# Kernel optimization log

Measured on AMD Instinct MI355X. Metric: run time of the kernel, lower is better.

Reference implementation:

```python
import jax, jax.numpy as jnp
import numpy as np
from jax import lax

K_NN = 16      # neighbors used by compute_knn_distance
ANCHOR_K = 64  # config['anchor_k']


def _knn_dist_vec(pts):
    """compute_knn_distance for one object: mean offset vector to K_NN nearest neighbors.
    pts: (N, 3) -> (N, 3)"""
    sq = jnp.sum(pts * pts, axis=-1)                      # (N,)
    d2 = sq[:, None] + sq[None, :] - 2.0 * (pts @ pts.T)  # (N, N) squared dists
    n = pts.shape[0]
    d2 = d2 + jnp.eye(n, dtype=pts.dtype) * 1e10          # exclude self
    _, idx = lax.top_k(-d2, K_NN)                          # (N, K_NN) nearest indices
    neigh = pts[idx]                                       # (N, K_NN, 3)
    return jnp.mean(neigh - pts[:, None, :], axis=1)       # (N, 3)


def _fps(pts, k):
    """Farthest point sampling for one object. pts: (N, 3) -> (k,) int32 indices."""
    d0 = jnp.sum((pts - pts[0]) ** 2, axis=-1)             # dist to seed point 0

    def step(min_d, _):
        idx = jnp.argmax(min_d)
        d = jnp.sum((pts - pts[idx]) ** 2, axis=-1)
        return jnp.minimum(min_d, d), idx

    _, idxs = lax.scan(step, d0, None, length=k - 1)
    return jnp.concatenate([jnp.zeros((1,), dtype=idxs.dtype), idxs])


def setup_inputs() -> dict:
    key = jax.random.key(0)
    k1, k2, k3, k4 = jax.random.split(key, 4)
    B, N_obj, N_v = 4, 8, 2048
    positions = jax.random.normal(k1, (B, N_obj, N_v, 3), dtype=jnp.float32)
    velocities = jax.random.normal(k2, (B, N_obj, N_v, 3), dtype=jnp.float32)
    physics_params = jax.random.uniform(k3, (B, N_obj, 3), dtype=jnp.float32)
    # reference pose at t=0: nearby but distinct so rel_pos is nontrivial
    ref_positions = positions + 0.05 * jax.random.normal(k4, (B, N_obj, N_v, 3), dtype=jnp.float32)
    return {"positions": positions, "velocities": velocities,
            "physics_params": physics_params, "ref_positions": ref_positions}


def reference(positions, velocities, physics_params, ref_positions):
    B, N_obj, N_v, _ = positions.shape
    flat = positions.reshape(B * N_obj, N_v, 3)

    # pairwise KNN distance feature per point
    dist_vec = jax.vmap(_knn_dist_vec)(flat).reshape(B, N_obj, N_v, 3)

    # iterative FPS anchor sampling (vectorized over all B*N_obj objects)
    anchors = jax.vmap(lambda p: _fps(p, ANCHOR_K))(flat).reshape(B, N_obj, ANCHOR_K)

    rel_pos = positions - ref_positions

    # multi-field gather at anchor indices (torch.gather on dim=2)
    gather = lambda f: jnp.take_along_axis(f, anchors[..., None], axis=2)
    anchor_dist = gather(dist_vec)       # (B, N_obj, K, 3)
    anchor_vel = gather(velocities)      # (B, N_obj, K, 3)
    anchor_rel = gather(rel_pos)         # (B, N_obj, K, 3)

    phys = jnp.broadcast_to(physics_params[:, :, None, :], (B, N_obj, ANCHOR_K, 3))
    query = jnp.concatenate([anchor_dist, anchor_vel, anchor_rel, phys], axis=-1)  # (B, N_obj, K, 12)
    return query
```

## Files before the change

kernel.cpp:

```cpp
#include <hip/hip_runtime.h>
#include <stdint.h>

#define NPTS 2048
#define KNN  16
#define AK   64
#define TPB  256
#define FPT  8
#define FPP  4
#define KPL  32
#define KPP  16

typedef unsigned long long u64;
typedef unsigned int u32;
typedef __attribute__((ext_vector_type(2))) float v2f;
#define UMAX 0xFFFFFFFFFFFFFFFFull

__device__ __forceinline__ float sq3(float x, float y, float z) {
    return __fadd_rn(__fadd_rn(__fmul_rn(x, x), __fmul_rn(y, y)), __fmul_rn(z, z));
}

template <int CTRL, int RMASK>
__device__ __forceinline__ u32 dpp32(u32 v) {
    return (u32)__builtin_amdgcn_update_dpp((int)v, (int)v, CTRL, RMASK, 0xF, false);
}

#define FMAX_STEP(CTRL, RMASK) \
    m = fmaxf(m, __uint_as_float(dpp32<CTRL, RMASK>(__float_as_uint(m))))
#define UMIN_STEP(CTRL, RMASK) \
    { const u32 o_ = dpp32<CTRL, RMASK>(c); c = (o_ < c) ? o_ : c; }

__device__ __forceinline__ float wave_fmax(float m) {
    FMAX_STEP(0xB1, 0xF);
    FMAX_STEP(0x4E, 0xF);
    FMAX_STEP(0x141, 0xF);
    FMAX_STEP(0x140, 0xF);
    FMAX_STEP(0x142, 0xA);
    FMAX_STEP(0x143, 0xC);
    return __uint_as_float((u32)__builtin_amdgcn_readlane(
        (int)__float_as_uint(m), 63));
}

__device__ __forceinline__ u32 wave_umin(u32 c) {
    UMIN_STEP(0xB1, 0xF);
    UMIN_STEP(0x4E, 0xF);
    UMIN_STEP(0x141, 0xF);
    UMIN_STEP(0x140, 0xF);
    UMIN_STEP(0x142, 0xA);
    UMIN_STEP(0x143, 0xC);
    return (u32)__builtin_amdgcn_readlane((int)c, 63);
}

template <int CTRL, int RMASK>
__device__ __forceinline__ u64 minstep(u64 k) {
    const u32 olo = dpp32<CTRL, RMASK>((u32)k);
    const u32 ohi = dpp32<CTRL, RMASK>((u32)(k >> 32));
    const u64 o = ((u64)ohi << 32) | olo;
    return (o < k) ? o : k;
}

__device__ __forceinline__ u64 wave_min64(u64 k) {
    k = minstep<0xB1, 0xF>(k);
    k = minstep<0x4E, 0xF>(k);
    k = minstep<0x141, 0xF>(k);
    k = minstep<0x140, 0xF>(k);
    k = minstep<0x142, 0xA>(k);
    k = minstep<0x143, 0xC>(k);
    const u32 lo = (u32)__builtin_amdgcn_readlane((int)(u32)k, 63);
    const u32 hi = (u32)__builtin_amdgcn_readlane((int)(u32)(k >> 32), 63);
    return ((u64)hi << 32) | lo;
}

__global__ __launch_bounds__(TPB) void fps_kernel(const float* __restrict__ pos,
                                                  int* __restrict__ anchors) {
#pragma clang fp contract(off)
    const int obj = blockIdx.x;
    const int t = threadIdx.x;
    const int wid = t >> 6;
    const float* pts = pos + (size_t)obj * NPTS * 3;

    __shared__ u64 skey[8];
    __shared__ float4 scrd[8];

    v2f px[FPP], py[FPP], pz[FPP], mind[FPP];
    float bv, bx, by, bz;
    u32 bj;
    {
        const float ax0 = pts[0], ay0 = pts[1], az0 = pts[2];
        bv = -1.0f; bj = 0; bx = by = bz = 0.0f;
        #pragma unroll
        for (int i = 0; i < FPP; i++) {
            const int jA = t + (2 * i) * TPB;
            const int jB = t + (2 * i + 1) * TPB;
            v2f X, Y, Z;
            X.x = pts[jA * 3 + 0]; Y.x = pts[jA * 3 + 1]; Z.x = pts[jA * 3 + 2];
            X.y = pts[jB * 3 + 0]; Y.y = pts[jB * 3 + 1]; Z.y = pts[jB * 3 + 2];
            px[i] = X; py[i] = Y; pz[i] = Z;
            const v2f dx = X - ax0, dy = Y - ay0, dz = Z - az0;
            const v2f d2 = dx * dx + dy * dy + dz * dz;
            mind[i] = d2;
            if (d2.x > bv) { bv = d2.x; bj = (u32)jA; bx = X.x; by = Y.x; bz = Z.x; }
            if (d2.y > bv) { bv = d2.y; bj = (u32)jB; bx = X.y; by = Y.y; bz = Z.y; }
        }
    }
    if (t == 0) anchors[obj * AK + 0] = 0;

    for (int s = 1; s < AK; s++) {
        const float wmax = wave_fmax(bv);
        const u32 cand = (bv == wmax) ? bj : 0xFFFFFFFFu;
        const u32 wj = wave_umin(cand);

        const int side = (s & 1) * 4;
        if (bv == wmax && bj == wj) {
            skey[side + wid] = ((u64)__float_as_uint(wmax) << 32) | (u32)(~wj);
            scrd[side + wid] = make_float4(bx, by, bz, 0.0f);
        }
        __syncthreads();

        u64 ka = skey[side + 0];
        float4 ca = scrd[side + 0];
        { const u64 kb = skey[side + 1]; const float4 cb = scrd[side + 1];
          if (kb > ka) { ka = kb; ca = cb; } }
        { const u64 kb = skey[side + 2]; const float4 cb = scrd[side + 2];
          if (kb > ka) { ka = kb; ca = cb; } }
        { const u64 kb = skey[side + 3]; const float4 cb = scrd[side + 3];
          if (kb > ka) { ka = kb; ca = cb; } }
        if (t == 0) anchors[obj * AK + s] = (int)(~(u32)ka);
        if (s == AK - 1) break;

        bv = -1.0f; bj = 0;
        #pragma unroll
        for (int i = 0; i < FPP; i++) {
            const v2f dx = px[i] - ca.x, dy = py[i] - ca.y, dz = pz[i] - ca.z;
            const v2f d2 = dx * dx + dy * dy + dz * dz;
            v2f nm;
            nm.x = fminf(mind[i].x, d2.x);
            nm.y = fminf(mind[i].y, d2.y);
            mind[i] = nm;
            if (nm.x > bv) { bv = nm.x; bj = (u32)(t + (2 * i) * TPB);
                             bx = px[i].x; by = py[i].x; bz = pz[i].x; }
            if (nm.y > bv) { bv = nm.y; bj = (u32)(t + (2 * i + 1) * TPB);
                             bx = px[i].y; by = py[i].y; bz = pz[i].y; }
        }
    }
}

__global__ __launch_bounds__(TPB) void knn_gather_kernel(
    const float* __restrict__ pos, const float* __restrict__ vel,
    const float* __restrict__ phys, const float* __restrict__ refp,
    const int* __restrict__ anchors, float* __restrict__ out) {
#pragma clang fp contract(off)
    const int t = threadIdx.x;
    const int wid = t >> 6, lane = t & 63;
    const int g = blockIdx.x * 4 + wid;
    const int obj = g >> 6;

    __shared__ float sX[NPTS], sY[NPTS], sZ[NPTS];
    const float* pts = pos + (size_t)obj * NPTS * 3;
    #pragma unroll
    for (int i = 0; i < FPT; i++) {
        const int j = t + i * TPB;
        sX[j] = pts[j * 3 + 0];
        sY[j] = pts[j * 3 + 1];
        sZ[j] = pts[j * 3 + 2];
    }
    const int a = anchors[g];
    __syncthreads();

    const float ax = sX[a], ay = sY[a], az = sZ[a];
    const float sqa = sq3(ax, ay, az);

    u64 k[KPL];
    #pragma unroll
    for (int i = 0; i < KPP; i++) {
        const int jA = lane + (2 * i) * 64, jB = lane + (2 * i + 1) * 64;
        v2f X, Y, Z;
        X.x = sX[jA]; Y.x = sY[jA]; Z.x = sZ[jA];
        X.y = sX[jB]; Y.y = sY[jB]; Z.y = sZ[jB];
        const v2f sqj = X * X + Y * Y + Z * Z;
        const v2f dot = ax * X + ay * Y + az * Z;
        const v2f d2 = (sqa + sqj) - 2.0f * dot;
        u32 b0 = __float_as_uint(d2.x);
        b0 ^= (b0 & 0x80000000u) ? 0xFFFFFFFFu : 0x80000000u;
        u32 b1 = __float_as_uint(d2.y);
        b1 ^= (b1 & 0x80000000u) ? 0xFFFFFFFFu : 0x80000000u;
        k[2 * i]     = (jA == a) ? UMAX : (((u64)b0 << 32) | (u32)jA);
        k[2 * i + 1] = (jB == a) ? UMAX : (((u64)b1 << 32) | (u32)jB);
    }

    u64 c0 = UMAX, c1 = UMAX;
    #pragma unroll
    for (int i = 0; i < KPL; i++) c0 = (k[i] < c0) ? k[i] : c0;
    #pragma unroll
    for (int i = 0; i < KPL; i++) {
        const u64 v = (k[i] > c0) ? k[i] : UMAX; c1 = (v < c1) ? v : c1;
    }

    float accx = 0.f, accy = 0.f, accz = 0.f;
    u64 thr = 0;
    for (int r = 0; r < KNN; r++) {
        if (c0 == UMAX) {
            #pragma unroll
            for (int i = 0; i < KPL; i++) {
                const u64 v = (k[i] > thr) ? k[i] : UMAX; c0 = (v < c0) ? v : c0;
            }
            #pragma unroll
            for (int i = 0; i < KPL; i++) {
                const u64 v = (k[i] > c0) ? k[i] : UMAX; c1 = (v < c1) ? v : c1;
            }
        }
        const u64 w = wave_min64(c0);
        const int winj = (int)(u32)w;
        accx = __fadd_rn(accx, __fsub_rn(sX[winj], ax));
        accy = __fadd_rn(accy, __fsub_rn(sY[winj], ay));
        accz = __fadd_rn(accz, __fsub_rn(sZ[winj], az));
        if (c0 == w) {
            thr = c0; c0 = c1; c1 = UMAX;
        }
    }

    if (lane == 0) {
        float* o = out + (size_t)g * 12;
        o[0] = __fmul_rn(accx, 0.0625f);
        o[1] = __fmul_rn(accy, 0.0625f);
        o[2] = __fmul_rn(accz, 0.0625f);
        const size_t base = (size_t)obj * NPTS * 3 + (size_t)a * 3;
        o[3] = vel[base + 0];
        o[4] = vel[base + 1];
        o[5] = vel[base + 2];
        o[6] = __fsub_rn(pos[base + 0], refp[base + 0]);
        o[7] = __fsub_rn(pos[base + 1], refp[base + 1]);
        o[8] = __fsub_rn(pos[base + 2], refp[base + 2]);
        const float* ph = phys + (size_t)obj * 3;
        o[9]  = ph[0];
        o[10] = ph[1];
        o[11] = ph[2];
    }
}

extern "C" void kernel_launch(void* const* d_in, const int* in_sizes, int n_in,
                              void* d_out, int out_size, void* d_ws, size_t ws_size,
                              hipStream_t stream) {
    const float* pos  = (const float*)d_in[0];
    const float* vel  = (const float*)d_in[1];
    const float* phys = (const float*)d_in[2];
    const float* refp = (const float*)d_in[3];
    float* out = (float*)d_out;

    const int n_obj = in_sizes[2] / 3;
    int* anchors = (int*)d_ws;

    fps_kernel<<<n_obj, TPB, 0, stream>>>(pos, anchors);
    knn_gather_kernel<<<n_obj * AK / 4, TPB, 0, stream>>>(pos, vel, phys, refp,
                                                          anchors, out);
}
```

Baseline: 117.4 us.

## Run FPS with one wavefront per object, removing block-level barriers

The FPS kernel now uses a single 64-lane wave per object, so each lane holds 32 points in registers instead of 8. The per-step cross-wave argmax through shared memory and __syncthreads is replaced by pure wave reductions. The winning point's coordinates are fetched with readlane from whichever register slot holds them. This removes barrier and LDS latency from the 63 serial steps. In exchange each step does four times more distance work per lane on four times fewer threads, and register pressure rises.

```diff
diff --git a/kernel.cpp b/kernel.cpp
--- a/kernel.cpp
+++ b/kernel.cpp
@@ -6,7 +6,6 @@
 #define AK   64
 #define TPB  256
 #define FPT  8
-#define FPP  4
 #define KPL  32
 #define KPP  16
 
@@ -70,27 +69,27 @@
     return ((u64)hi << 32) | lo;
 }
 
-__global__ __launch_bounds__(TPB) void fps_kernel(const float* __restrict__ pos,
-                                                  int* __restrict__ anchors) {
+__device__ __forceinline__ float rdlane(float v, u32 l) {
+    return __uint_as_float(
+        (u32)__builtin_amdgcn_readlane((int)__float_as_uint(v), (int)l));
+}
+
+__global__ __launch_bounds__(64) void fps_kernel(const float* __restrict__ pos,
+                                                 int* __restrict__ anchors) {
 #pragma clang fp contract(off)
     const int obj = blockIdx.x;
-    const int t = threadIdx.x;
-    const int wid = t >> 6;
+    const int lane = threadIdx.x;
     const float* pts = pos + (size_t)obj * NPTS * 3;
 
-    __shared__ u64 skey[8];
-    __shared__ float4 scrd[8];
-
-    v2f px[FPP], py[FPP], pz[FPP], mind[FPP];
-    float bv, bx, by, bz;
-    u32 bj;
+    v2f px[KPP], py[KPP], pz[KPP], mind[KPP];
+    float bv = -1.0f;
+    u32 bj = 0;
     {
         const float ax0 = pts[0], ay0 = pts[1], az0 = pts[2];
-        bv = -1.0f; bj = 0; bx = by = bz = 0.0f;
         #pragma unroll
-        for (int i = 0; i < FPP; i++) {
-            const int jA = t + (2 * i) * TPB;
-            const int jB = t + (2 * i + 1) * TPB;
+        for (int i = 0; i < KPP; i++) {
+            const int jA = lane + (2 * i) * 64;
+            const int jB = lane + (2 * i + 1) * 64;
             v2f X, Y, Z;
             X.x = pts[jA * 3 + 0]; Y.x = pts[jA * 3 + 1]; Z.x = pts[jA * 3 + 2];
             X.y = pts[jB * 3 + 0]; Y.y = pts[jB * 3 + 1]; Z.y = pts[jB * 3 + 2];
@@ -98,48 +97,49 @@
             const v2f dx = X - ax0, dy = Y - ay0, dz = Z - az0;
             const v2f d2 = dx * dx + dy * dy + dz * dz;
             mind[i] = d2;
-            if (d2.x > bv) { bv = d2.x; bj = (u32)jA; bx = X.x; by = Y.x; bz = Z.x; }
-            if (d2.y > bv) { bv = d2.y; bj = (u32)jB; bx = X.y; by = Y.y; bz = Z.y; }
-        }
-    }
-    if (t == 0) anchors[obj * AK + 0] = 0;
+            if (d2.x > bv) { bv = d2.x; bj = (u32)jA; }
+            if (d2.y > bv) { bv = d2.y; bj = (u32)jB; }
+        }
+    }
+    if (lane == 0) anchors[obj * AK + 0] = 0;
 
     for (int s = 1; s < AK; s++) {
         const float wmax = wave_fmax(bv);
         const u32 cand = (bv == wmax) ? bj : 0xFFFFFFFFu;
         const u32 wj = wave_umin(cand);
-
-        const int side = (s & 1) * 4;
-        if (bv == wmax && bj == wj) {
-            skey[side + wid] = ((u64)__float_as_uint(wmax) << 32) | (u32)(~wj);
-            scrd[side + wid] = make_float4(bx, by, bz, 0.0f);
-        }
-        __syncthreads();
-
-        u64 ka = skey[side + 0];
-        float4 ca = scrd[side + 0];
-        { const u64 kb = skey[side + 1]; const float4 cb = scrd[side + 1];
-          if (kb > ka) { ka = kb; ca = cb; } }
-        { const u64 kb = skey[side + 2]; const float4 cb = scrd[side + 2];
-          if (kb > ka) { ka = kb; ca = cb; } }
-        { const u64 kb = skey[side + 3]; const float4 cb = scrd[side + 3];
-          if (kb > ka) { ka = kb; ca = cb; } }
-        if (t == 0) anchors[obj * AK + s] = (int)(~(u32)ka);
+        if (lane == 0) anchors[obj * AK + s] = (int)wj;
         if (s == AK - 1) break;
+
+        const u32 slot = wj >> 6;
+        const u32 wl = wj & 63u;
+        float cx = 0.f, cy = 0.f, cz = 0.f;
+        #pragma unroll
+        for (int i = 0; i < KPL; i++) {
+            if (slot == (u32)i) {
+                const int p = i >> 1;
+                if ((i & 1) == 0) {
+                    cx = rdlane(px[p].x, wl);
+                    cy = rdlane(py[p].x, wl);
+                    cz = rdlane(pz[p].x, wl);
+                } else {
+                    cx = rdlane(px[p].y, wl);
+                    cy = rdlane(py[p].y, wl);
+                    cz = rdlane(pz[p].y, wl);
+                }
+            }
+        }
 
         bv = -1.0f; bj = 0;
         #pragma unroll
-        for (int i = 0; i < FPP; i++) {
-            const v2f dx = px[i] - ca.x, dy = py[i] - ca.y, dz = pz[i] - ca.z;
+        for (int i = 0; i < KPP; i++) {
+            const v2f dx = px[i] - cx, dy = py[i] - cy, dz = pz[i] - cz;
             const v2f d2 = dx * dx + dy * dy + dz * dz;
             v2f nm;
             nm.x = fminf(mind[i].x, d2.x);
             nm.y = fminf(mind[i].y, d2.y);
             mind[i] = nm;
-            if (nm.x > bv) { bv = nm.x; bj = (u32)(t + (2 * i) * TPB);
-                             bx = px[i].x; by = py[i].x; bz = pz[i].x; }
-            if (nm.y > bv) { bv = nm.y; bj = (u32)(t + (2 * i + 1) * TPB);
-                             bx = px[i].y; by = py[i].y; bz = pz[i].y; }
+            if (nm.x > bv) { bv = nm.x; bj = (u32)(lane + (2 * i) * 64); }
+            if (nm.y > bv) { bv = nm.y; bj = (u32)(lane + (2 * i + 1) * 64); }
         }
     }
 }
@@ -249,7 +249,7 @@
     const int n_obj = in_sizes[2] / 3;
     int* anchors = (int*)d_ws;
 
-    fps_kernel<<<n_obj, TPB, 0, stream>>>(pos, anchors);
+    fps_kernel<<<n_obj, 64, 0, stream>>>(pos, anchors);
     knn_gather_kernel<<<n_obj * AK / 4, TPB, 0, stream>>>(pos, vel, phys, refp,
                                                           anchors, out);
 }
```

New measurement: 144.5 us. +23.1%, slower.

## Process four objects per FPS block to amortize barriers and reductions

Applied to the files above, without the earlier changes.

The FPS kernel now handles four objects per block, interleaving their independent wave reductions and distance updates so that one __syncthreads per step serves all four objects. This is meant to hide reduction and barrier latency through instruction-level parallelism. In exchange, register pressure roughly quadruples and the grid shrinks from 32 blocks to 8, which leaves many CUs idle. It also assumes the object count divides by four.

```diff
diff --git a/kernel.cpp b/kernel.cpp
--- a/kernel.cpp
+++ b/kernel.cpp
@@ -7,6 +7,7 @@
 #define TPB  256
 #define FPT  8
 #define FPP  4
+#define OPB  4
 #define KPL  32
 #define KPP  16
 
@@ -70,23 +71,25 @@
     return ((u64)hi << 32) | lo;
 }
 
-__global__ __launch_bounds__(TPB) void fps_kernel(const float* __restrict__ pos,
-                                                  int* __restrict__ anchors) {
+__global__ __launch_bounds__(TPB, 1) void fps_kernel(const float* __restrict__ pos,
+                                                     int* __restrict__ anchors) {
 #pragma clang fp contract(off)
-    const int obj = blockIdx.x;
+    const int ob = blockIdx.x * OPB;
     const int t = threadIdx.x;
     const int wid = t >> 6;
-    const float* pts = pos + (size_t)obj * NPTS * 3;
-
-    __shared__ u64 skey[8];
-    __shared__ float4 scrd[8];
-
-    v2f px[FPP], py[FPP], pz[FPP], mind[FPP];
-    float bv, bx, by, bz;
-    u32 bj;
-    {
+
+    __shared__ u64 skey[OPB][8];
+    __shared__ float4 scrd[OPB][8];
+
+    v2f px[OPB][FPP], py[OPB][FPP], pz[OPB][FPP], mind[OPB][FPP];
+    float bv[OPB], bx[OPB], by[OPB], bz[OPB];
+    u32 bj[OPB];
+
+    #pragma unroll
+    for (int o = 0; o < OPB; o++) {
+        const float* pts = pos + (size_t)(ob + o) * NPTS * 3;
         const float ax0 = pts[0], ay0 = pts[1], az0 = pts[2];
-        bv = -1.0f; bj = 0; bx = by = bz = 0.0f;
+        bv[o] = -1.0f; bj[o] = 0; bx[o] = by[o] = bz[o] = 0.0f;
         #pragma unroll
         for (int i = 0; i < FPP; i++) {
             const int jA = t + (2 * i) * TPB;
@@ -94,52 +97,65 @@
             v2f X, Y, Z;
             X.x = pts[jA * 3 + 0]; Y.x = pts[jA * 3 + 1]; Z.x = pts[jA * 3 + 2];
             X.y = pts[jB * 3 + 0]; Y.y = pts[jB * 3 + 1]; Z.y = pts[jB * 3 + 2];
-            px[i] = X; py[i] = Y; pz[i] = Z;
+            px[o][i] = X; py[o][i] = Y; pz[o][i] = Z;
             const v2f dx = X - ax0, dy = Y - ay0, dz = Z - az0;
             const v2f d2 = dx * dx + dy * dy + dz * dz;
-            mind[i] = d2;
-            if (d2.x > bv) { bv = d2.x; bj = (u32)jA; bx = X.x; by = Y.x; bz = Z.x; }
-            if (d2.y > bv) { bv = d2.y; bj = (u32)jB; bx = X.y; by = Y.y; bz = Z.y; }
-        }
-    }
-    if (t == 0) anchors[obj * AK + 0] = 0;
+            mind[o][i] = d2;
+            if (d2.x > bv[o]) { bv[o] = d2.x; bj[o] = (u32)jA;
+                                bx[o] = X.x; by[o] = Y.x; bz[o] = Z.x; }
+            if (d2.y > bv[o]) { bv[o] = d2.y; bj[o] = (u32)jB;
+                                bx[o] = X.y; by[o] = Y.y; bz[o] = Z.y; }
+        }
+        if (t == 0) anchors[(ob + o) * AK + 0] = 0;
+    }
 
     for (int s = 1; s < AK; s++) {
-        const float wmax = wave_fmax(bv);
-        const u32 cand = (bv == wmax) ? bj : 0xFFFFFFFFu;
-        const u32 wj = wave_umin(cand);
-
         const int side = (s & 1) * 4;
-        if (bv == wmax && bj == wj) {
-            skey[side + wid] = ((u64)__float_as_uint(wmax) << 32) | (u32)(~wj);
-            scrd[side + wid] = make_float4(bx, by, bz, 0.0f);
+
+        #pragma unroll
+        for (int o = 0; o < OPB; o++) {
+            const float wmax = wave_fmax(bv[o]);
+            const u32 cand = (bv[o] == wmax) ? bj[o] : 0xFFFFFFFFu;
+            const u32 wj = wave_umin(cand);
+            if (bv[o] == wmax && bj[o] == wj) {
+                skey[o][side + wid] = ((u64)__float_as_uint(wmax) << 32)
+                                      | (u32)(~wj);
+                scrd[o][side + wid] = make_float4(bx[o], by[o], bz[o], 0.0f);
+            }
         }
         __syncthreads();
 
-        u64 ka = skey[side + 0];
-        float4 ca = scrd[side + 0];
-        { const u64 kb = skey[side + 1]; const float4 cb = scrd[side + 1];
-          if (kb > ka) { ka = kb; ca = cb; } }
-        { const u64 kb = skey[side + 2]; const float4 cb = scrd[side + 2];
-          if (kb > ka) { ka = kb; ca = cb; } }
-        { const u64 kb = skey[side + 3]; const float4 cb = scrd[side + 3];
-          if (kb > ka) { ka = kb; ca = cb; } }
-        if (t == 0) anchors[obj * AK + s] = (int)(~(u32)ka);
-        if (s == AK - 1) break;
-
-        bv = -1.0f; bj = 0;
         #pragma unroll
-        for (int i = 0; i < FPP; i++) {
-            const v2f dx = px[i] - ca.x, dy = py[i] - ca.y, dz = pz[i] - ca.z;
-            const v2f d2 = dx * dx + dy * dy + dz * dz;
-            v2f nm;
-            nm.x = fminf(mind[i].x, d2.x);
-            nm.y = fminf(mind[i].y, d2.y);
-            mind[i] = nm;
-            if (nm.x > bv) { bv = nm.x; bj = (u32)(t + (2 * i) * TPB);
-                             bx = px[i].x; by = py[i].x; bz = pz[i].x; }
-            if (nm.y > bv) { bv = nm.y; bj = (u32)(t + (2 * i + 1) * TPB);
-                             bx = px[i].y; by = py[i].y; bz = pz[i].y; }
+        for (int o = 0; o < OPB; o++) {
+            u64 ka = skey[o][side + 0];
+            float4 ca = scrd[o][side + 0];
+            { const u64 kb = skey[o][side + 1]; const float4 cb = scrd[o][side + 1];
+              if (kb > ka) { ka = kb; ca = cb; } }
+            { const u64 kb = skey[o][side + 2]; const float4 cb = scrd[o][side + 2];
+              if (kb > ka) { ka = kb; ca = cb; } }
+            { const u64 kb = skey[o][side + 3]; const float4 cb = scrd[o][side + 3];
+              if (kb > ka) { ka = kb; ca = cb; } }
+            if (t == 0) anchors[(ob + o) * AK + s] = (int)(~(u32)ka);
+            if (s == AK - 1) continue;
+
+            bv[o] = -1.0f; bj[o] = 0;
+            #pragma unroll
+            for (int i = 0; i < FPP; i++) {
+                const v2f dx = px[o][i] - ca.x, dy = py[o][i] - ca.y,
+                          dz = pz[o][i] - ca.z;
+                const v2f d2 = dx * dx + dy * dy + dz * dz;
+                v2f nm;
+                nm.x = fminf(mind[o][i].x, d2.x);
+                nm.y = fminf(mind[o][i].y, d2.y);
+                mind[o][i] = nm;
+                if (nm.x > bv[o]) { bv[o] = nm.x; bj[o] = (u32)(t + (2 * i) * TPB);
+                                    bx[o] = px[o][i].x; by[o] = py[o][i].x;
+                                    bz[o] = pz[o][i].x; }
+                if (nm.y > bv[o]) { bv[o] = nm.y;
+                                    bj[o] = (u32)(t + (2 * i + 1) * TPB);
+                                    bx[o] = px[o][i].y; by[o] = py[o][i].y;
+                                    bz[o] = pz[o][i].y; }
+            }
         }
     }
 }
@@ -249,7 +265,7 @@
     const int n_obj = in_sizes[2] / 3;
     int* anchors = (int*)d_ws;
 
-    fps_kernel<<<n_obj, TPB, 0, stream>>>(pos, anchors);
+    fps_kernel<<<n_obj / OPB, TPB, 0, stream>>>(pos, anchors);
     knn_gather_kernel<<<n_obj * AK / 4, TPB, 0, stream>>>(pos, vel, phys, refp,
                                                           anchors, out);
 }
```

Result: slower. 231.2 us (+96.9%).
